# Performance work log

Hardware: AMD Instinct MI355X
Metric: run time of the kernel (lower is better)

Reference implementation:

```python
import jax, jax.numpy as jnp
import numpy as np

MODEL_DIM = 2048
NUM_HEADS = 16
HEAD_DIM = MODEL_DIM // NUM_HEADS  # 128
B, L = 2, 2048


def _rope_tables(seq_len, head_dim, theta=10000.0):
    inv = 1.0 / (theta ** (np.arange(0, head_dim, 2)[: head_dim // 2].astype(np.float32) / head_dim))
    t = np.arange(seq_len, dtype=np.float32)
    freqs = np.outer(t, inv)  # [L, head_dim//2]
    return jnp.asarray(np.cos(freqs)), jnp.asarray(np.sin(freqs))


def setup_inputs() -> dict:
    key = jax.random.key(0)
    k1, k2, k3 = jax.random.split(key, 3)
    x = jax.random.normal(k1, (B, L, MODEL_DIM), dtype=jnp.float32)
    Wqkv = jax.random.normal(k2, (MODEL_DIM, 3 * MODEL_DIM), dtype=jnp.float32) / np.sqrt(MODEL_DIM)
    Wc = jax.random.normal(k3, (MODEL_DIM, MODEL_DIM), dtype=jnp.float32) / np.sqrt(MODEL_DIM)
    bc = jnp.zeros((MODEL_DIM,), dtype=jnp.float32)
    freqs_cos, freqs_sin = _rope_tables(L, HEAD_DIM)
    return {"x": x, "freqs_cos": freqs_cos, "freqs_sin": freqs_sin,
            "Wqkv": Wqkv, "Wc": Wc, "bc": bc}


def _apply_rope(t, cos, sin):
    # t: [B, L, H, hd] viewed as pairs (even, odd) along last dim; complex multiply by cis
    b, l, h, d = t.shape
    tp = t.reshape(b, l, h, d // 2, 2)
    te, to = tp[..., 0], tp[..., 1]
    cos = cos[None, :, None, :]  # [1, L, 1, d/2]
    sin = sin[None, :, None, :]
    oe = te * cos - to * sin
    oo = te * sin + to * cos
    return jnp.stack([oe, oo], axis=-1).reshape(b, l, h, d)


def reference(x, freqs_cos, freqs_sin, Wqkv, Wc, bc):
    b, l, d = x.shape
    qkv = x @ Wqkv  # [B, L, 3D]
    q, k, v = jnp.split(qkv, 3, axis=-1)
    q = q.reshape(b, l, NUM_HEADS, HEAD_DIM)
    k = k.reshape(b, l, NUM_HEADS, HEAD_DIM)
    v = v.reshape(b, l, NUM_HEADS, HEAD_DIM)
    q = _apply_rope(q, freqs_cos, freqs_sin)
    k = _apply_rope(k, freqs_cos, freqs_sin)
    scale = 1.0 / np.sqrt(HEAD_DIM).astype(np.float32)
    # causal SDPA: [B, H, Lq, Lk]
    scores = jnp.einsum('bqhd,bkhd->bhqk', q, k) * scale
    causal = jnp.tril(jnp.ones((l, l), dtype=bool))
    scores = jnp.where(causal[None, None], scores, jnp.finfo(scores.dtype).min)
    attn = jax.nn.softmax(scores, axis=-1)
    out = jnp.einsum('bhqk,bkhd->bqhd', attn, v).reshape(b, l, d)
    return out @ Wc + bc
```

## Files before the change

kernel.cpp:

```cpp
#include <hip/hip_runtime.h>
#include <hip/hip_bf16.h>

#define MODEL 2048
#define NHEAD 16
#define HDIM  128
#define BB    2
#define LL    2048
#define N1    (3*MODEL)
#define MTOT  (BB*LL)

typedef __hip_bfloat16 bf16;
typedef __attribute__((ext_vector_type(8))) short bf16x8;
typedef __attribute__((ext_vector_type(4))) float f32x4;

static __device__ __forceinline__ f32x4 mfma16(bf16x8 a, bf16x8 b, f32x4 c) {
  return __builtin_amdgcn_mfma_f32_16x16x32_bf16(a, b, c, 0, 0, 0);
}

static __device__ __forceinline__ void gl_lds16(const void* g, void* l) {
  __builtin_amdgcn_global_load_lds(
      (const __attribute__((address_space(1))) unsigned int*)g,
      (__attribute__((address_space(3))) unsigned int*)l, 16, 0, 0);
}

static __device__ __forceinline__ unsigned bfu(float x) {
  bf16 b = __float2bfloat16(x);
  return (unsigned)*reinterpret_cast<unsigned short*>(&b);
}

#define BARRIER __builtin_amdgcn_s_barrier()
#define SCHED0  __builtin_amdgcn_sched_barrier(0)
#define PRIO1 __builtin_amdgcn_s_setprio(1)
#define PRIO0 __builtin_amdgcn_s_setprio(0)

__global__ void k_cvt(const float* __restrict__ in, bf16* __restrict__ out, int n4) {
  int i = blockIdx.x * blockDim.x + threadIdx.x;
  if (i < n4) {
    float4 v = ((const float4*)in)[i];
    bf16* o = out + (size_t)i * 4;
    o[0] = __float2bfloat16(v.x);
    o[1] = __float2bfloat16(v.y);
    o[2] = __float2bfloat16(v.z);
    o[3] = __float2bfloat16(v.w);
  }
}

__global__ __launch_bounds__(256)
void k_transpose(const float* __restrict__ in, bf16* __restrict__ out, int R, int C) {
  __shared__ float t[32][33];
  const int c0 = blockIdx.x * 32, r0 = blockIdx.y * 32;
  const int tx = threadIdx.x & 31;
  const int ty = threadIdx.x >> 5;
#pragma unroll
  for (int i = 0; i < 4; ++i)
    t[ty + 8*i][tx] = in[(size_t)(r0 + ty + 8*i) * C + c0 + tx];
  __syncthreads();
#pragma unroll
  for (int i = 0; i < 4; ++i)
    out[(size_t)(c0 + ty + 8*i) * R + r0 + tx] = __float2bfloat16(t[tx][ty + 8*i]);
}

template<int EPI>
__global__ __launch_bounds__(512, 4)
void k_gemmP(const bf16* __restrict__ A, const bf16* __restrict__ BT,
             int M, int N, int K,
             float* __restrict__ Cout, const float* __restrict__ bias,
             bf16* __restrict__ Qb, bf16* __restrict__ Kb, bf16* __restrict__ VTb,
             const float* __restrict__ cosT, const float* __restrict__ sinT)
{
  constexpr int ABUF = 8192;
  constexpr int BBUF = 8192;
  constexpr int AREG = 3 * ABUF;
  extern __shared__ char smem[];

  const int tid = threadIdx.x;
  const int wid = tid >> 6, lane = tid & 63;
  const int wm = wid >> 2, wn = wid & 3;
  const int lr = lane & 15, lkg = lane >> 4;

  const int nbx = N >> 7;
  const int xcd = blockIdx.x & 7;
  const int i   = blockIdx.x >> 3;
  const int m0 = (((xcd >> 1) << 3) + (i & 7)) << 7;
  const int n0 = ((xcd & 1) * (nbx >> 1) + (i >> 3)) << 7;

  const int scol = ((lane & 3) ^ ((lane >> 3) & 3)) * 8;
  const bf16* Asrc = A  + (size_t)(m0 + wid*16 + (lane >> 2)) * K + scol;
  const bf16* Bsrc = BT + (size_t)(n0 + wid*16 + (lane >> 2)) * K + scol;

  auto stageA = [&](int t) {
    gl_lds16(Asrc + t*32, smem + (t % 3)*ABUF + wid*1024);
  };
  auto stageB = [&](int t) {
    gl_lds16(Bsrc + t*32, smem + AREG + (t % 3)*BBUF + wid*1024);
  };

  const int slotX = (lkg ^ ((lr >> 1) & 3)) * 16;
  const int aBase = wm*4096 + lr*64 + slotX;
  const int bBase = wn*2048 + lr*64 + slotX;

  const f32x4 vzero = {0.f, 0.f, 0.f, 0.f};
  f32x4 acc[4][2];
#pragma unroll
  for (int ii = 0; ii < 4; ++ii)
#pragma unroll
    for (int j = 0; j < 2; ++j) acc[ii][j] = vzero;

  const int nt = K >> 5;

  stageA(0); stageB(0); stageA(1); stageB(1);
  asm volatile("s_waitcnt vmcnt(2)" ::: "memory");
  SCHED0; BARRIER;

  for (int t = 0; t < nt; ++t) {
    const int bufA = (t % 3) * ABUF;
    const int bufB = AREG + (t % 3) * BBUF;
    const int ts   = (t + 2 < nt) ? t + 2 : nt - 1;
    bf16x8 aFr[4], bFr[2];

#pragma unroll
    for (int mf = 0; mf < 4; ++mf)
      aFr[mf] = *(const bf16x8*)(smem + bufA + aBase + mf*1024);
#pragma unroll
    for (int nf = 0; nf < 2; ++nf)
      bFr[nf] = *(const bf16x8*)(smem + bufB + bBase + nf*1024);
    stageA(ts); stageB(ts);

    PRIO1;
#pragma unroll
    for (int mf = 0; mf < 4; ++mf)
#pragma unroll
      for (int nf = 0; nf < 2; ++nf)
        acc[mf][nf] = mfma16(aFr[mf], bFr[nf], acc[mf][nf]);
    PRIO0;
    asm volatile("s_waitcnt vmcnt(2)" ::: "memory");
    SCHED0;
    BARRIER;
  }

  if constexpr (EPI == 1) {
    const float inv_sqrt_d = 0.08838834764831845f;
#pragma unroll
    for (int nf = 0; nf < 2; ++nf) {
      const int gcb = n0 + wn*32 + nf*16;
      const int section = gcb >> 11;
      const int cc = (gcb & 2047) + lr;
      const int h = cc >> 7, d = cc & 127;
#pragma unroll
      for (int mf = 0; mf < 4; ++mf) {
#pragma unroll
        for (int reg = 0; reg < 4; ++reg) {
          const int grow = m0 + wm*64 + mf*16 + lkg*4 + reg;
          const int bidx = grow >> 11, lseq = grow & 2047;
          float val = acc[mf][nf][reg];
          if (section < 2) {
            float p = __shfl_xor(val, 1);
            const int fi = d >> 1;
            float cv = cosT[(size_t)lseq * 64 + fi];
            float sv = sinT[(size_t)lseq * 64 + fi];
            float r = (d & 1) ? fmaf(p, sv, val * cv)
                              : fmaf(val, cv, -p * sv);
            if (section == 0) {
              r *= inv_sqrt_d;
              Qb[((size_t)(bidx*NHEAD + h) * LL + lseq) * HDIM + d] = __float2bfloat16(r);
            } else {
              Kb[((size_t)(bidx*NHEAD + h) * LL + lseq) * HDIM + d] = __float2bfloat16(r);
            }
          } else {
            VTb[((size_t)(bidx*NHEAD + h) * HDIM + d) * LL + lseq] = __float2bfloat16(val);
          }
        }
      }
    }
  } else {
#pragma unroll
    for (int nf = 0; nf < 2; ++nf) {
      const int gcol = n0 + wn*32 + nf*16 + lr;
      const float bv = bias[gcol];
#pragma unroll
      for (int mf = 0; mf < 4; ++mf) {
#pragma unroll
        for (int reg = 0; reg < 4; ++reg) {
          const int grow = m0 + wm*64 + mf*16 + lkg*4 + reg;
          Cout[(size_t)grow * N + gcol] = acc[mf][nf][reg] + bv;
        }
      }
    }
  }
}

__global__ __launch_bounds__(256, 2)
void k_attn(const bf16* __restrict__ Qb, const bf16* __restrict__ Kb,
            const bf16* __restrict__ VTb, bf16* __restrict__ attnA)
{
  __shared__ bf16 Ks[64][136];
  __shared__ bf16 Vs[128][72];
  __shared__ bf16 Ps[4][32][72];

  const int bh  = blockIdx.y;
  const int bx  = blockIdx.x;
  const int tid = threadIdx.x;
  const int wid = tid >> 6, lane = tid & 63;
  const int lr  = lane & 15, lkg = lane >> 4;

  const bf16* Qh = Qb  + (size_t)bh * LL * HDIM;
  const bf16* Kh = Kb  + (size_t)bh * LL * HDIM;
  const bf16* Vh = VTb + (size_t)bh * HDIM * LL;
  const int b = bh >> 4, h = bh & 15;
  const f32x4 vzero = {0.f, 0.f, 0.f, 0.f};

  for (int pp = 0; pp < 2; ++pp) {
    const int qt  = pp ? bx : (15 - bx);
    const int Q0  = qt * 128;
    const int q0w = Q0 + wid * 32;

    bf16x8 qf[2][4];
#pragma unroll
    for (int qr = 0; qr < 2; ++qr)
#pragma unroll
      for (int kk = 0; kk < 4; ++kk)
        qf[qr][kk] = *(const bf16x8*)(Qh + (size_t)(q0w + qr*16 + lr) * HDIM + kk*32 + lkg*8);

    f32x4 oacc[2][8];
#pragma unroll
    for (int qr = 0; qr < 2; ++qr)
#pragma unroll
      for (int db = 0; db < 8; ++db) oacc[qr][db] = vzero;
    float ml[2] = {-INFINITY, -INFINITY};
    float ll[2] = {0.f, 0.f};

    const int NT = Q0 / 64 + 2;
    bf16x8 kpre[4], vpre[4];
#pragma unroll
    for (int j = 0; j < 4; ++j) {
      const int c = j*256 + tid;
      kpre[j] = *(const bf16x8*)(Kh + (size_t)(c >> 4) * HDIM + (c & 15) * 8);
      vpre[j] = *(const bf16x8*)(Vh + (size_t)(c >> 3) * LL + (c & 7) * 8);
    }

    for (int kt = 0; kt < NT; ++kt) {
      const int kbase = kt * 64;
      __syncthreads();
#pragma unroll
      for (int j = 0; j < 4; ++j) {
        const int c = j*256 + tid;
        *(bf16x8*)&Ks[c >> 4][(c & 15) * 8] = kpre[j];
        *(bf16x8*)&Vs[c >> 3][(c & 7) * 8]  = vpre[j];
      }
      __syncthreads();
      if (kt + 1 < NT) {
#pragma unroll
        for (int j = 0; j < 4; ++j) {
          const int c = j*256 + tid;
          kpre[j] = *(const bf16x8*)(Kh + (size_t)((kt+1)*64 + (c >> 4)) * HDIM + (c & 15) * 8);
          vpre[j] = *(const bf16x8*)(Vh + (size_t)(c >> 3) * LL + (kt+1)*64 + (c & 7) * 8);
        }
      }
      if (kbase <= q0w + 31) {
        f32x4 s2[2][4];
#pragma unroll
        for (int qr = 0; qr < 2; ++qr)
#pragma unroll
          for (int c = 0; c < 4; ++c) s2[qr][c] = vzero;
#pragma unroll
        for (int c = 0; c < 4; ++c) {
          bf16x8 kf[4];
#pragma unroll
          for (int kk = 0; kk < 4; ++kk)
            kf[kk] = *(const bf16x8*)&Ks[c*16 + lr][kk*32 + lkg*8];
#pragma unroll
          for (int qr = 0; qr < 2; ++qr)
#pragma unroll
            for (int kk = 0; kk < 4; ++kk)
              s2[qr][c] = mfma16(kf[kk], qf[qr][kk], s2[qr][c]);
        }
#pragma unroll
        for (int qr = 0; qr < 2; ++qr) {
          const int qrow = q0w + qr*16 + lr;
          float pv[4][4];
#pragma unroll
          for (int c = 0; c < 4; ++c)
#pragma unroll
            for (int reg = 0; reg < 4; ++reg) {
              const int kv = kbase + c*16 + lkg*4 + reg;
              pv[c][reg] = (kv <= qrow) ? s2[qr][c][reg] : -INFINITY;
            }
          float tm = pv[0][0];
#pragma unroll
          for (int c = 0; c < 4; ++c)
#pragma unroll
            for (int reg = 0; reg < 4; ++reg)
              if (c || reg) tm = fmaxf(tm, pv[c][reg]);
          tm = fmaxf(tm, __shfl_xor(tm, 16));
          tm = fmaxf(tm, __shfl_xor(tm, 32));
          const float mnew = fmaxf(ml[qr], tm);
          const float scl  = __expf(ml[qr] - mnew);
          ml[qr] = mnew;
          float rs = 0.f;
#pragma unroll
          for (int c = 0; c < 4; ++c)
#pragma unroll
            for (int reg = 0; reg < 4; ++reg) {
              pv[c][reg] = __expf(pv[c][reg] - mnew);
              rs += pv[c][reg];
            }
          rs += __shfl_xor(rs, 16);
          rs += __shfl_xor(rs, 32);
          ll[qr] = ll[qr] * scl + rs;
#pragma unroll
          for (int c = 0; c < 4; ++c) {
            unsigned lo = bfu(pv[c][0]) | (bfu(pv[c][1]) << 16);
            unsigned hi = bfu(pv[c][2]) | (bfu(pv[c][3]) << 16);
            *(uint2*)&Ps[wid][qr*16 + lr][c*16 + lkg*4] = make_uint2(lo, hi);
          }
          float sr[4];
#pragma unroll
          for (int reg = 0; reg < 4; ++reg) sr[reg] = __shfl(scl, lkg*4 + reg);
#pragma unroll
          for (int db = 0; db < 8; ++db) {
            oacc[qr][db][0] *= sr[0]; oacc[qr][db][1] *= sr[1];
            oacc[qr][db][2] *= sr[2]; oacc[qr][db][3] *= sr[3];
          }
        }
        asm volatile("s_waitcnt lgkmcnt(0)" ::: "memory");
        __builtin_amdgcn_sched_barrier(0);
        bf16x8 pf[2][2];
#pragma unroll
        for (int qr = 0; qr < 2; ++qr)
#pragma unroll
          for (int k2 = 0; k2 < 2; ++k2)
            pf[qr][k2] = *(const bf16x8*)&Ps[wid][qr*16 + lr][k2*32 + lkg*8];
#pragma unroll
        for (int db = 0; db < 8; ++db) {
          bf16x8 vf0 = *(const bf16x8*)&Vs[db*16 + lr][lkg*8];
          bf16x8 vf1 = *(const bf16x8*)&Vs[db*16 + lr][32 + lkg*8];
#pragma unroll
          for (int qr = 0; qr < 2; ++qr) {
            oacc[qr][db] = mfma16(pf[qr][0], vf0, oacc[qr][db]);
            oacc[qr][db] = mfma16(pf[qr][1], vf1, oacc[qr][db]);
          }
        }
      }
    }

#pragma unroll
    for (int qr = 0; qr < 2; ++qr) {
      const float myinv = 1.0f / ll[qr];
      float li[4];
#pragma unroll
      for (int reg = 0; reg < 4; ++reg) li[reg] = __shfl(myinv, lkg*4 + reg);
#pragma unroll
      for (int reg = 0; reg < 4; ++reg) {
        const int row = q0w + qr*16 + lkg*4 + reg;
        bf16* dst = attnA + ((size_t)(b*LL + row)) * MODEL + h * HDIM;
#pragma unroll
        for (int db = 0; db < 8; ++db)
          dst[db*16 + lr] = __float2bfloat16(oacc[qr][db][reg] * li[reg]);
      }
    }
  }
}

extern "C" void kernel_launch(void* const* d_in, const int* in_sizes, int n_in,
                              void* d_out, int out_size, void* d_ws, size_t ws_size,
                              hipStream_t stream)
{
  const float* x    = (const float*)d_in[0];
  const float* cosT = (const float*)d_in[1];
  const float* sinT = (const float*)d_in[2];
  const float* Wqkv = (const float*)d_in[3];
  const float* Wc   = (const float*)d_in[4];
  const float* bc   = (const float*)d_in[5];
  float* out = (float*)d_out;

  if (ws_size < 100663296u) return;
  char* w = (char*)d_ws;
  bf16* x16   = (bf16*)(w);
  bf16* WqkvT = (bf16*)(w + (size_t)16777216);
  bf16* WcT   = (bf16*)(w + (size_t)41943040);
  bf16* Qb    = (bf16*)(w + (size_t)50331648);
  bf16* Kb    = (bf16*)(w + (size_t)67108864);
  bf16* VTb   = (bf16*)(w + (size_t)83886080);
  bf16* attnA = x16;

  hipFuncSetAttribute(reinterpret_cast<const void*>(&k_gemmP<1>),
                      hipFuncAttributeMaxDynamicSharedMemorySize, 49152);
  hipFuncSetAttribute(reinterpret_cast<const void*>(&k_gemmP<2>),
                      hipFuncAttributeMaxDynamicSharedMemorySize, 49152);

  k_cvt<<<(MTOT*MODEL/4 + 255)/256, 256, 0, stream>>>(x, x16, MTOT*MODEL/4);
  k_transpose<<<dim3(N1/32,    MODEL/32), 256, 0, stream>>>(Wqkv, WqkvT, MODEL, N1);
  k_transpose<<<dim3(MODEL/32, MODEL/32), 256, 0, stream>>>(Wc,   WcT,   MODEL, MODEL);

  k_gemmP<1><<<(N1/128)*(MTOT/128), 512, 49152, stream>>>(
      x16, WqkvT, MTOT, N1, MODEL,
      nullptr, nullptr, Qb, Kb, VTb, cosT, sinT);

  k_attn<<<dim3(8, BB*NHEAD), 256, 0, stream>>>(Qb, Kb, VTb, attnA);

  k_gemmP<2><<<(MODEL/128)*(MTOT/128), 512, 49152, stream>>>(
      attnA, WcT, MTOT, MODEL, MODEL,
      out, bc, nullptr, nullptr, nullptr, nullptr, nullptr);
}
```

Baseline: 296.7 us.

## Use 4-wave GEMM blocks with 64x64 warp tiles and double buffering

```diff
diff --git a/kernel.cpp b/kernel.cpp
--- a/kernel.cpp
+++ b/kernel.cpp
@@ -61,21 +61,18 @@
 }
 
 template<int EPI>
-__global__ __launch_bounds__(512, 4)
+__global__ __launch_bounds__(256, 5)
 void k_gemmP(const bf16* __restrict__ A, const bf16* __restrict__ BT,
              int M, int N, int K,
              float* __restrict__ Cout, const float* __restrict__ bias,
              bf16* __restrict__ Qb, bf16* __restrict__ Kb, bf16* __restrict__ VTb,
              const float* __restrict__ cosT, const float* __restrict__ sinT)
 {
-  constexpr int ABUF = 8192;
-  constexpr int BBUF = 8192;
-  constexpr int AREG = 3 * ABUF;
   extern __shared__ char smem[];
 
   const int tid = threadIdx.x;
   const int wid = tid >> 6, lane = tid & 63;
-  const int wm = wid >> 2, wn = wid & 3;
+  const int wm = wid >> 1, wn = wid & 1;
   const int lr = lane & 15, lkg = lane >> 4;
 
   const int nbx = N >> 7;
@@ -85,55 +82,58 @@
   const int n0 = ((xcd & 1) * (nbx >> 1) + (i >> 3)) << 7;
 
   const int scol = ((lane & 3) ^ ((lane >> 3) & 3)) * 8;
-  const bf16* Asrc = A  + (size_t)(m0 + wid*16 + (lane >> 2)) * K + scol;
-  const bf16* Bsrc = BT + (size_t)(n0 + wid*16 + (lane >> 2)) * K + scol;
-
-  auto stageA = [&](int t) {
-    gl_lds16(Asrc + t*32, smem + (t % 3)*ABUF + wid*1024);
-  };
-  auto stageB = [&](int t) {
-    gl_lds16(Bsrc + t*32, smem + AREG + (t % 3)*BBUF + wid*1024);
+  const bf16* Asrc = A  + (size_t)(m0 + wid*32 + (lane >> 2)) * K + scol;
+  const bf16* Bsrc = BT + (size_t)(n0 + wid*32 + (lane >> 2)) * K + scol;
+
+  auto stage = [&](int t) {
+    const bf16* ga = Asrc + t*32;
+    const bf16* gb = Bsrc + t*32;
+    char* da = smem + (t & 1)*16384 + wid*2048;
+    char* db = smem + (t & 1)*16384 + 8192 + wid*2048;
+    gl_lds16(ga,                da);
+    gl_lds16(ga + (size_t)16*K, da + 1024);
+    gl_lds16(gb,                db);
+    gl_lds16(gb + (size_t)16*K, db + 1024);
   };
 
   const int slotX = (lkg ^ ((lr >> 1) & 3)) * 16;
   const int aBase = wm*4096 + lr*64 + slotX;
-  const int bBase = wn*2048 + lr*64 + slotX;
+  const int bBase = 8192 + wn*4096 + lr*64 + slotX;
 
   const f32x4 vzero = {0.f, 0.f, 0.f, 0.f};
-  f32x4 acc[4][2];
+  f32x4 acc[4][4];
 #pragma unroll
   for (int ii = 0; ii < 4; ++ii)
 #pragma unroll
-    for (int j = 0; j < 2; ++j) acc[ii][j] = vzero;
+    for (int j = 0; j < 4; ++j) acc[ii][j] = vzero;
 
   const int nt = K >> 5;
 
-  stageA(0); stageB(0); stageA(1); stageB(1);
-  asm volatile("s_waitcnt vmcnt(2)" ::: "memory");
+  stage(0);
+  asm volatile("s_waitcnt vmcnt(0)" ::: "memory");
   SCHED0; BARRIER;
 
   for (int t = 0; t < nt; ++t) {
-    const int bufA = (t % 3) * ABUF;
-    const int bufB = AREG + (t % 3) * BBUF;
-    const int ts   = (t + 2 < nt) ? t + 2 : nt - 1;
-    bf16x8 aFr[4], bFr[2];
+    const int buf = (t & 1) * 16384;
+    bf16x8 aFr[4], bFr[4];
+
+    if (t + 1 < nt) stage(t + 1);
 
 #pragma unroll
     for (int mf = 0; mf < 4; ++mf)
-      aFr[mf] = *(const bf16x8*)(smem + bufA + aBase + mf*1024);
-#pragma unroll
-    for (int nf = 0; nf < 2; ++nf)
-      bFr[nf] = *(const bf16x8*)(smem + bufB + bBase + nf*1024);
-    stageA(ts); stageB(ts);
+      aFr[mf] = *(const bf16x8*)(smem + buf + aBase + mf*1024);
+#pragma unroll
+    for (int nf = 0; nf < 4; ++nf)
+      bFr[nf] = *(const bf16x8*)(smem + buf + bBase + nf*1024);
 
     PRIO1;
 #pragma unroll
     for (int mf = 0; mf < 4; ++mf)
 #pragma unroll
-      for (int nf = 0; nf < 2; ++nf)
+      for (int nf = 0; nf < 4; ++nf)
         acc[mf][nf] = mfma16(aFr[mf], bFr[nf], acc[mf][nf]);
     PRIO0;
-    asm volatile("s_waitcnt vmcnt(2)" ::: "memory");
+    asm volatile("s_waitcnt vmcnt(0)" ::: "memory");
     SCHED0;
     BARRIER;
   }
@@ -141,8 +141,8 @@
   if constexpr (EPI == 1) {
     const float inv_sqrt_d = 0.08838834764831845f;
 #pragma unroll
-    for (int nf = 0; nf < 2; ++nf) {
-      const int gcb = n0 + wn*32 + nf*16;
+    for (int nf = 0; nf < 4; ++nf) {
+      const int gcb = n0 + wn*64 + nf*16;
       const int section = gcb >> 11;
       const int cc = (gcb & 2047) + lr;
       const int h = cc >> 7, d = cc & 127;
@@ -174,8 +174,8 @@
     }
   } else {
 #pragma unroll
-    for (int nf = 0; nf < 2; ++nf) {
-      const int gcol = n0 + wn*32 + nf*16 + lr;
+    for (int nf = 0; nf < 4; ++nf) {
+      const int gcol = n0 + wn*64 + nf*16 + lr;
       const float bv = bias[gcol];
 #pragma unroll
       for (int mf = 0; mf < 4; ++mf) {
@@ -384,21 +384,21 @@
   bf16* attnA = x16;
 
   hipFuncSetAttribute(reinterpret_cast<const void*>(&k_gemmP<1>),
-                      hipFuncAttributeMaxDynamicSharedMemorySize, 49152);
+                      hipFuncAttributeMaxDynamicSharedMemorySize, 32768);
   hipFuncSetAttribute(reinterpret_cast<const void*>(&k_gemmP<2>),
-                      hipFuncAttributeMaxDynamicSharedMemorySize, 49152);
+                      hipFuncAttributeMaxDynamicSharedMemorySize, 32768);
 
   k_cvt<<<(MTOT*MODEL/4 + 255)/256, 256, 0, stream>>>(x, x16, MTOT*MODEL/4);
   k_transpose<<<dim3(N1/32,    MODEL/32), 256, 0, stream>>>(Wqkv, WqkvT, MODEL, N1);
   k_transpose<<<dim3(MODEL/32, MODEL/32), 256, 0, stream>>>(Wc,   WcT,   MODEL, MODEL);
 
-  k_gemmP<1><<<(N1/128)*(MTOT/128), 512, 49152, stream>>>(
+  k_gemmP<1><<<(N1/128)*(MTOT/128), 256, 32768, stream>>>(
       x16, WqkvT, MTOT, N1, MODEL,
       nullptr, nullptr, Qb, Kb, VTb, cosT, sinT);
 
   k_attn<<<dim3(8, BB*NHEAD), 256, 0, stream>>>(Qb, Kb, VTb, attnA);
 
-  k_gemmP<2><<<(MODEL/128)*(MTOT/128), 512, 49152, stream>>>(
+  k_gemmP<2><<<(MODEL/128)*(MTOT/128), 256, 32768, stream>>>(
       attnA, WcT, MTOT, MODEL, MODEL,
       out, bc, nullptr, nullptr, nullptr, nullptr, nullptr);
 }
```

Measured after the change: 679.3 us. +128.9%, slower.

## Fuse fp32-to-bf16 conversion of x into the QKV GEMM A-tile loading

Applied to the files above, without the earlier changes.

```diff
diff --git a/kernel.cpp b/kernel.cpp
--- a/kernel.cpp
+++ b/kernel.cpp
@@ -23,27 +23,18 @@
       (__attribute__((address_space(3))) unsigned int*)l, 16, 0, 0);
 }
 
+static __device__ __forceinline__ unsigned short bfraw(float x) {
+  bf16 b = __float2bfloat16(x);
+  return *reinterpret_cast<unsigned short*>(&b);
+}
 static __device__ __forceinline__ unsigned bfu(float x) {
-  bf16 b = __float2bfloat16(x);
-  return (unsigned)*reinterpret_cast<unsigned short*>(&b);
+  return (unsigned)bfraw(x);
 }
 
 #define BARRIER __builtin_amdgcn_s_barrier()
 #define SCHED0  __builtin_amdgcn_sched_barrier(0)
 #define PRIO1 __builtin_amdgcn_s_setprio(1)
 #define PRIO0 __builtin_amdgcn_s_setprio(0)
-
-__global__ void k_cvt(const float* __restrict__ in, bf16* __restrict__ out, int n4) {
-  int i = blockIdx.x * blockDim.x + threadIdx.x;
-  if (i < n4) {
-    float4 v = ((const float4*)in)[i];
-    bf16* o = out + (size_t)i * 4;
-    o[0] = __float2bfloat16(v.x);
-    o[1] = __float2bfloat16(v.y);
-    o[2] = __float2bfloat16(v.z);
-    o[3] = __float2bfloat16(v.w);
-  }
-}
 
 __global__ __launch_bounds__(256)
 void k_transpose(const float* __restrict__ in, bf16* __restrict__ out, int R, int C) {
@@ -62,7 +53,7 @@
 
 template<int EPI>
 __global__ __launch_bounds__(512, 4)
-void k_gemmP(const bf16* __restrict__ A, const bf16* __restrict__ BT,
+void k_gemmP(const void* __restrict__ Ain, const bf16* __restrict__ BT,
              int M, int N, int K,
              float* __restrict__ Cout, const float* __restrict__ bias,
              bf16* __restrict__ Qb, bf16* __restrict__ Kb, bf16* __restrict__ VTb,
@@ -81,20 +72,44 @@
   const int nbx = N >> 7;
   const int xcd = blockIdx.x & 7;
   const int i   = blockIdx.x >> 3;
-  const int m0 = (((xcd >> 1) << 3) + (i & 7)) << 7;
-  const int n0 = ((xcd & 1) * (nbx >> 1) + (i >> 3)) << 7;
+  int m0, n0;
+  if constexpr (EPI == 1) {
+    m0 = ((xcd << 2) + (i & 3)) << 7;
+    n0 = (i >> 2) << 7;
+  } else {
+    m0 = (((xcd >> 1) << 3) + (i & 7)) << 7;
+    n0 = ((xcd & 1) * (nbx >> 1) + (i >> 3)) << 7;
+  }
 
   const int scol = ((lane & 3) ^ ((lane >> 3) & 3)) * 8;
-  const bf16* Asrc = A  + (size_t)(m0 + wid*16 + (lane >> 2)) * K + scol;
   const bf16* Bsrc = BT + (size_t)(n0 + wid*16 + (lane >> 2)) * K + scol;
-
-  auto stageA = [&](int t) {
-    gl_lds16(Asrc + t*32, smem + (t % 3)*ABUF + wid*1024);
-  };
   auto stageB = [&](int t) {
     gl_lds16(Bsrc + t*32, smem + AREG + (t % 3)*BBUF + wid*1024);
   };
 
+  const bf16*  AsrcH = (const bf16*)Ain;
+  const float* AsrcF = (const float*)Ain;
+  const bf16*  AsrcB = AsrcH + (size_t)(m0 + wid*16 + (lane >> 2)) * K + scol;
+  const float* AsrcX = AsrcF + (size_t)(m0 + wid*16 + (lane >> 2)) * K + (lane & 3) * 8;
+  const int awAddr = (wid*16 + (lane >> 2)) * 64 + ((lane & 3) ^ ((lane >> 3) & 3)) * 16;
+
+  float4 rA0, rA1;
+  auto loadAf = [&](int t) {
+    rA0 = *(const float4*)(AsrcX + (size_t)t * 32);
+    rA1 = *(const float4*)(AsrcX + (size_t)t * 32 + 4);
+  };
+  auto writeA = [&](int tbuf) {
+    union { bf16x8 v; unsigned short s[8]; } u;
+    u.s[0] = bfraw(rA0.x); u.s[1] = bfraw(rA0.y);
+    u.s[2] = bfraw(rA0.z); u.s[3] = bfraw(rA0.w);
+    u.s[4] = bfraw(rA1.x); u.s[5] = bfraw(rA1.y);
+    u.s[6] = bfraw(rA1.z); u.s[7] = bfraw(rA1.w);
+    *(bf16x8*)(smem + (tbuf % 3)*ABUF + awAddr) = u.v;
+  };
+  auto stageA_bf = [&](int t) {
+    gl_lds16(AsrcB + t*32, smem + (t % 3)*ABUF + wid*1024);
+  };
+
   const int slotX = (lkg ^ ((lr >> 1) & 3)) * 16;
   const int aBase = wm*4096 + lr*64 + slotX;
   const int bBase = wn*2048 + lr*64 + slotX;
@@ -108,14 +123,24 @@
 
   const int nt = K >> 5;
 
-  stageA(0); stageB(0); stageA(1); stageB(1);
-  asm volatile("s_waitcnt vmcnt(2)" ::: "memory");
+  if constexpr (EPI == 1) {
+    loadAf(0);
+    stageB(0); stageB(1);
+    writeA(0);
+    loadAf(1);
+    writeA(1);
+    loadAf(2);
+    asm volatile("s_waitcnt vmcnt(3) lgkmcnt(0)" ::: "memory");
+  } else {
+    stageA_bf(0); stageB(0); stageA_bf(1); stageB(1);
+    asm volatile("s_waitcnt vmcnt(2)" ::: "memory");
+  }
   SCHED0; BARRIER;
 
   for (int t = 0; t < nt; ++t) {
     const int bufA = (t % 3) * ABUF;
     const int bufB = AREG + (t % 3) * BBUF;
-    const int ts   = (t + 2 < nt) ? t + 2 : nt - 1;
+    const int t2 = (t + 2 < nt) ? t + 2 : nt - 1;
     bf16x8 aFr[4], bFr[2];
 
 #pragma unroll
@@ -124,7 +149,15 @@
 #pragma unroll
     for (int nf = 0; nf < 2; ++nf)
       bFr[nf] = *(const bf16x8*)(smem + bufB + bBase + nf*1024);
-    stageA(ts); stageB(ts);
+
+    if constexpr (EPI == 1) {
+      writeA(t + 2);
+      stageB(t2);
+      const int t3 = (t + 3 < nt) ? t + 3 : nt - 1;
+      loadAf(t3);
+    } else {
+      stageA_bf(t2); stageB(t2);
+    }
 
     PRIO1;
 #pragma unroll
@@ -133,7 +166,11 @@
       for (int nf = 0; nf < 2; ++nf)
         acc[mf][nf] = mfma16(aFr[mf], bFr[nf], acc[mf][nf]);
     PRIO0;
-    asm volatile("s_waitcnt vmcnt(2)" ::: "memory");
+    if constexpr (EPI == 1) {
+      asm volatile("s_waitcnt vmcnt(3) lgkmcnt(0)" ::: "memory");
+    } else {
+      asm volatile("s_waitcnt vmcnt(2)" ::: "memory");
+    }
     SCHED0;
     BARRIER;
   }
@@ -375,25 +412,23 @@
 
   if (ws_size < 100663296u) return;
   char* w = (char*)d_ws;
-  bf16* x16   = (bf16*)(w);
+  bf16* attnA = (bf16*)(w);
   bf16* WqkvT = (bf16*)(w + (size_t)16777216);
   bf16* WcT   = (bf16*)(w + (size_t)41943040);
   bf16* Qb    = (bf16*)(w + (size_t)50331648);
   bf16* Kb    = (bf16*)(w + (size_t)67108864);
   bf16* VTb   = (bf16*)(w + (size_t)83886080);
-  bf16* attnA = x16;
 
   hipFuncSetAttribute(reinterpret_cast<const void*>(&k_gemmP<1>),
                       hipFuncAttributeMaxDynamicSharedMemorySize, 49152);
   hipFuncSetAttribute(reinterpret_cast<const void*>(&k_gemmP<2>),
                       hipFuncAttributeMaxDynamicSharedMemorySize, 49152);
 
-  k_cvt<<<(MTOT*MODEL/4 + 255)/256, 256, 0, stream>>>(x, x16, MTOT*MODEL/4);
   k_transpose<<<dim3(N1/32,    MODEL/32), 256, 0, stream>>>(Wqkv, WqkvT, MODEL, N1);
   k_transpose<<<dim3(MODEL/32, MODEL/32), 256, 0, stream>>>(Wc,   WcT,   MODEL, MODEL);
 
   k_gemmP<1><<<(N1/128)*(MTOT/128), 512, 49152, stream>>>(
-      x16, WqkvT, MTOT, N1, MODEL,
+      x, WqkvT, MTOT, N1, MODEL,
       nullptr, nullptr, Qb, Kb, VTb, cosT, sinT);
 
   k_attn<<<dim3(8, BB*NHEAD), 256, 0, stream>>>(Qb, Kb, VTb, attnA);
```

After: 302.1 us. About the same (+1.8%).

## Process both paired causal query tiles concurrently with 512-thread attention blocks

Applied to the files above, without the earlier changes.

```diff
diff --git a/kernel.cpp b/kernel.cpp
--- a/kernel.cpp
+++ b/kernel.cpp
@@ -189,13 +189,14 @@
   }
 }
 
-__global__ __launch_bounds__(256, 2)
+__global__ __launch_bounds__(512)
 void k_attn(const bf16* __restrict__ Qb, const bf16* __restrict__ Kb,
             const bf16* __restrict__ VTb, bf16* __restrict__ attnA)
 {
-  __shared__ bf16 Ks[64][136];
-  __shared__ bf16 Vs[128][72];
-  __shared__ bf16 Ps[4][32][72];
+  extern __shared__ char asmem[];
+  bf16* Ks = (bf16*)asmem;
+  bf16* Vs = (bf16*)(asmem + 17408);
+  bf16* Ps = (bf16*)(asmem + 17408 + 18432);
 
   const int bh  = blockIdx.y;
   const int bx  = blockIdx.x;
@@ -209,154 +210,152 @@
   const int b = bh >> 4, h = bh & 15;
   const f32x4 vzero = {0.f, 0.f, 0.f, 0.f};
 
-  for (int pp = 0; pp < 2; ++pp) {
-    const int qt  = pp ? bx : (15 - bx);
-    const int Q0  = qt * 128;
-    const int q0w = Q0 + wid * 32;
-
-    bf16x8 qf[2][4];
-#pragma unroll
-    for (int qr = 0; qr < 2; ++qr)
-#pragma unroll
-      for (int kk = 0; kk < 4; ++kk)
-        qf[qr][kk] = *(const bf16x8*)(Qh + (size_t)(q0w + qr*16 + lr) * HDIM + kk*32 + lkg*8);
-
-    f32x4 oacc[2][8];
-#pragma unroll
-    for (int qr = 0; qr < 2; ++qr)
-#pragma unroll
-      for (int db = 0; db < 8; ++db) oacc[qr][db] = vzero;
-    float ml[2] = {-INFINITY, -INFINITY};
-    float ll[2] = {0.f, 0.f};
-
-    const int NT = Q0 / 64 + 2;
-    bf16x8 kpre[4], vpre[4];
-#pragma unroll
-    for (int j = 0; j < 4; ++j) {
-      const int c = j*256 + tid;
-      kpre[j] = *(const bf16x8*)(Kh + (size_t)(c >> 4) * HDIM + (c & 15) * 8);
-      vpre[j] = *(const bf16x8*)(Vh + (size_t)(c >> 3) * LL + (c & 7) * 8);
-    }
-
-    for (int kt = 0; kt < NT; ++kt) {
-      const int kbase = kt * 64;
-      __syncthreads();
-#pragma unroll
-      for (int j = 0; j < 4; ++j) {
-        const int c = j*256 + tid;
-        *(bf16x8*)&Ks[c >> 4][(c & 15) * 8] = kpre[j];
-        *(bf16x8*)&Vs[c >> 3][(c & 7) * 8]  = vpre[j];
-      }
-      __syncthreads();
-      if (kt + 1 < NT) {
-#pragma unroll
-        for (int j = 0; j < 4; ++j) {
-          const int c = j*256 + tid;
-          kpre[j] = *(const bf16x8*)(Kh + (size_t)((kt+1)*64 + (c >> 4)) * HDIM + (c & 15) * 8);
-          vpre[j] = *(const bf16x8*)(Vh + (size_t)(c >> 3) * LL + (kt+1)*64 + (c & 7) * 8);
+  const int qt  = (wid < 4) ? (15 - bx) : bx;
+  const int q0w = qt * 128 + (wid & 3) * 32;
+
+  bf16x8 qf[2][4];
+#pragma unroll
+  for (int qr = 0; qr < 2; ++qr)
+#pragma unroll
+    for (int kk = 0; kk < 4; ++kk)
+      qf[qr][kk] = *(const bf16x8*)(Qh + (size_t)(q0w + qr*16 + lr) * HDIM + kk*32 + lkg*8);
+
+  f32x4 oacc[2][8];
+#pragma unroll
+  for (int qr = 0; qr < 2; ++qr)
+#pragma unroll
+    for (int db = 0; db < 8; ++db) oacc[qr][db] = vzero;
+  float ml[2] = {-INFINITY, -INFINITY};
+  float ll[2] = {0.f, 0.f};
+
+  const int NT = (15 - bx) * 2 + 2;
+
+  bf16x8 kpre[2], vpre[2];
+#pragma unroll
+  for (int j = 0; j < 2; ++j) {
+    const int c = j*512 + tid;
+    kpre[j] = *(const bf16x8*)(Kh + (size_t)(c >> 4) * HDIM + (c & 15) * 8);
+    vpre[j] = *(const bf16x8*)(Vh + (size_t)(c >> 3) * LL + (c & 7) * 8);
+  }
+
+  for (int kt = 0; kt < NT; ++kt) {
+    const int kbase = kt * 64;
+    __syncthreads();
+#pragma unroll
+    for (int j = 0; j < 2; ++j) {
+      const int c = j*512 + tid;
+      *(bf16x8*)&Ks[(c >> 4) * 136 + (c & 15) * 8] = kpre[j];
+      *(bf16x8*)&Vs[(c >> 3) * 72  + (c & 7)  * 8] = vpre[j];
+    }
+    __syncthreads();
+    if (kt + 1 < NT) {
+#pragma unroll
+      for (int j = 0; j < 2; ++j) {
+        const int c = j*512 + tid;
+        kpre[j] = *(const bf16x8*)(Kh + (size_t)((kt+1)*64 + (c >> 4)) * HDIM + (c & 15) * 8);
+        vpre[j] = *(const bf16x8*)(Vh + (size_t)(c >> 3) * LL + (kt+1)*64 + (c & 7) * 8);
+      }
+    }
+    if (kbase <= q0w + 31) {
+      f32x4 s2[2][4];
+#pragma unroll
+      for (int qr = 0; qr < 2; ++qr)
+#pragma unroll
+        for (int c = 0; c < 4; ++c) s2[qr][c] = vzero;
+#pragma unroll
+      for (int c = 0; c < 4; ++c) {
+        bf16x8 kf[4];
+#pragma unroll
+        for (int kk = 0; kk < 4; ++kk)
+          kf[kk] = *(const bf16x8*)&Ks[(c*16 + lr) * 136 + kk*32 + lkg*8];
+#pragma unroll
+        for (int qr = 0; qr < 2; ++qr)
+#pragma unroll
+          for (int kk = 0; kk < 4; ++kk)
+            s2[qr][c] = mfma16(kf[kk], qf[qr][kk], s2[qr][c]);
+      }
+#pragma unroll
+      for (int qr = 0; qr < 2; ++qr) {
+        const int qrow = q0w + qr*16 + lr;
+        float pv[4][4];
+#pragma unroll
+        for (int c = 0; c < 4; ++c)
+#pragma unroll
+          for (int reg = 0; reg < 4; ++reg) {
+            const int kv = kbase + c*16 + lkg*4 + reg;
+            pv[c][reg] = (kv <= qrow) ? s2[qr][c][reg] : -INFINITY;
+          }
+        float tm = pv[0][0];
+#pragma unroll
+        for (int c = 0; c < 4; ++c)
+#pragma unroll
+          for (int reg = 0; reg < 4; ++reg)
+            if (c || reg) tm = fmaxf(tm, pv[c][reg]);
+        tm = fmaxf(tm, __shfl_xor(tm, 16));
+        tm = fmaxf(tm, __shfl_xor(tm, 32));
+        const float mnew = fmaxf(ml[qr], tm);
+        const float scl  = __expf(ml[qr] - mnew);
+        ml[qr] = mnew;
+        float rs = 0.f;
+#pragma unroll
+        for (int c = 0; c < 4; ++c)
+#pragma unroll
+          for (int reg = 0; reg < 4; ++reg) {
+            pv[c][reg] = __expf(pv[c][reg] - mnew);
+            rs += pv[c][reg];
+          }
+        rs += __shfl_xor(rs, 16);
+        rs += __shfl_xor(rs, 32);
+        ll[qr] = ll[qr] * scl + rs;
+#pragma unroll
+        for (int c = 0; c < 4; ++c) {
+          unsigned lo = bfu(pv[c][0]) | (bfu(pv[c][1]) << 16);
+          unsigned hi = bfu(pv[c][2]) | (bfu(pv[c][3]) << 16);
+          *(uint2*)&Ps[(wid*32 + qr*16 + lr) * 72 + c*16 + lkg*4] = make_uint2(lo, hi);
         }
-      }
-      if (kbase <= q0w + 31) {
-        f32x4 s2[2][4];
-#pragma unroll
-        for (int qr = 0; qr < 2; ++qr)
-#pragma unroll
-          for (int c = 0; c < 4; ++c) s2[qr][c] = vzero;
-#pragma unroll
-        for (int c = 0; c < 4; ++c) {
-          bf16x8 kf[4];
-#pragma unroll
-          for (int kk = 0; kk < 4; ++kk)
-            kf[kk] = *(const bf16x8*)&Ks[c*16 + lr][kk*32 + lkg*8];
-#pragma unroll
-          for (int qr = 0; qr < 2; ++qr)
-#pragma unroll
-            for (int kk = 0; kk < 4; ++kk)
-              s2[qr][c] = mfma16(kf[kk], qf[qr][kk], s2[qr][c]);
+        float sr[4];
+#pragma unroll
+        for (int reg = 0; reg < 4; ++reg) sr[reg] = __shfl(scl, lkg*4 + reg);
+#pragma unroll
+        for (int db = 0; db < 8; ++db) {
+          oacc[qr][db][0] *= sr[0]; oacc[qr][db][1] *= sr[1];
+          oacc[qr][db][2] *= sr[2]; oacc[qr][db][3] *= sr[3];
         }
+      }
+      asm volatile("s_waitcnt lgkmcnt(0)" ::: "memory");
+      __builtin_amdgcn_sched_barrier(0);
+      bf16x8 pf[2][2];
+#pragma unroll
+      for (int qr = 0; qr < 2; ++qr)
+#pragma unroll
+        for (int k2 = 0; k2 < 2; ++k2)
+          pf[qr][k2] = *(const bf16x8*)&Ps[(wid*32 + qr*16 + lr) * 72 + k2*32 + lkg*8];
+#pragma unroll
+      for (int db = 0; db < 8; ++db) {
+        bf16x8 vf0 = *(const bf16x8*)&Vs[(db*16 + lr) * 72 + lkg*8];
+        bf16x8 vf1 = *(const bf16x8*)&Vs[(db*16 + lr) * 72 + 32 + lkg*8];
 #pragma unroll
         for (int qr = 0; qr < 2; ++qr) {
-          const int qrow = q0w + qr*16 + lr;
-          float pv[4][4];
-#pragma unroll
-          for (int c = 0; c < 4; ++c)
-#pragma unroll
-            for (int reg = 0; reg < 4; ++reg) {
-              const int kv = kbase + c*16 + lkg*4 + reg;
-              pv[c][reg] = (kv <= qrow) ? s2[qr][c][reg] : -INFINITY;
-            }
-          float tm = pv[0][0];
-#pragma unroll
-          for (int c = 0; c < 4; ++c)
-#pragma unroll
-            for (int reg = 0; reg < 4; ++reg)
-              if (c || reg) tm = fmaxf(tm, pv[c][reg]);
-          tm = fmaxf(tm, __shfl_xor(tm, 16));
-          tm = fmaxf(tm, __shfl_xor(tm, 32));
-          const float mnew = fmaxf(ml[qr], tm);
-          const float scl  = __expf(ml[qr] - mnew);
-          ml[qr] = mnew;
-          float rs = 0.f;
-#pragma unroll
-          for (int c = 0; c < 4; ++c)
-#pragma unroll
-            for (int reg = 0; reg < 4; ++reg) {
-              pv[c][reg] = __expf(pv[c][reg] - mnew);
-              rs += pv[c][reg];
-            }
-          rs += __shfl_xor(rs, 16);
-          rs += __shfl_xor(rs, 32);
-          ll[qr] = ll[qr] * scl + rs;
-#pragma unroll
-          for (int c = 0; c < 4; ++c) {
-            unsigned lo = bfu(pv[c][0]) | (bfu(pv[c][1]) << 16);
-            unsigned hi = bfu(pv[c][2]) | (bfu(pv[c][3]) << 16);
-            *(uint2*)&Ps[wid][qr*16 + lr][c*16 + lkg*4] = make_uint2(lo, hi);
-          }
-          float sr[4];
-#pragma unroll
-          for (int reg = 0; reg < 4; ++reg) sr[reg] = __shfl(scl, lkg*4 + reg);
-#pragma unroll
-          for (int db = 0; db < 8; ++db) {
-            oacc[qr][db][0] *= sr[0]; oacc[qr][db][1] *= sr[1];
-            oacc[qr][db][2] *= sr[2]; oacc[qr][db][3] *= sr[3];
-          }
+          oacc[qr][db] = mfma16(pf[qr][0], vf0, oacc[qr][db]);
+          oacc[qr][db] = mfma16(pf[qr][1], vf1, oacc[qr][db]);
         }
-        asm volatile("s_waitcnt lgkmcnt(0)" ::: "memory");
-        __builtin_amdgcn_sched_barrier(0);
-        bf16x8 pf[2][2];
-#pragma unroll
-        for (int qr = 0; qr < 2; ++qr)
-#pragma unroll
-          for (int k2 = 0; k2 < 2; ++k2)
-            pf[qr][k2] = *(const bf16x8*)&Ps[wid][qr*16 + lr][k2*32 + lkg*8];
-#pragma unroll
-        for (int db = 0; db < 8; ++db) {
-          bf16x8 vf0 = *(const bf16x8*)&Vs[db*16 + lr][lkg*8];
-          bf16x8 vf1 = *(const bf16x8*)&Vs[db*16 + lr][32 + lkg*8];
-#pragma unroll
-          for (int qr = 0; qr < 2; ++qr) {
-            oacc[qr][db] = mfma16(pf[qr][0], vf0, oacc[qr][db]);
-            oacc[qr][db] = mfma16(pf[qr][1], vf1, oacc[qr][db]);
-          }
-        }
-      }
-    }
-
-#pragma unroll
-    for (int qr = 0; qr < 2; ++qr) {
-      const float myinv = 1.0f / ll[qr];
-      float li[4];
-#pragma unroll
-      for (int reg = 0; reg < 4; ++reg) li[reg] = __shfl(myinv, lkg*4 + reg);
-#pragma unroll
-      for (int reg = 0; reg < 4; ++reg) {
-        const int row = q0w + qr*16 + lkg*4 + reg;
-        bf16* dst = attnA + ((size_t)(b*LL + row)) * MODEL + h * HDIM;
-#pragma unroll
-        for (int db = 0; db < 8; ++db)
-          dst[db*16 + lr] = __float2bfloat16(oacc[qr][db][reg] * li[reg]);
-      }
+      }
+    }
+  }
+
+#pragma unroll
+  for (int qr = 0; qr < 2; ++qr) {
+    const float myinv = 1.0f / ll[qr];
+    float li[4];
+#pragma unroll
+    for (int reg = 0; reg < 4; ++reg) li[reg] = __shfl(myinv, lkg*4 + reg);
+#pragma unroll
+    for (int reg = 0; reg < 4; ++reg) {
+      const int row = q0w + qr*16 + lkg*4 + reg;
+      bf16* dst = attnA + ((size_t)(b*LL + row)) * MODEL + h * HDIM;
+#pragma unroll
+      for (int db = 0; db < 8; ++db)
+        dst[db*16 + lr] = __float2bfloat16(oacc[qr][db][reg] * li[reg]);
     }
   }
 }
@@ -387,6 +386,8 @@
                       hipFuncAttributeMaxDynamicSharedMemorySize, 49152);
   hipFuncSetAttribute(reinterpret_cast<const void*>(&k_gemmP<2>),
                       hipFuncAttributeMaxDynamicSharedMemorySize, 49152);
+  hipFuncSetAttribute(reinterpret_cast<const void*>(&k_attn),
+                      hipFuncAttributeMaxDynamicSharedMemorySize, 73728);
 
   k_cvt<<<(MTOT*MODEL/4 + 255)/256, 256, 0, stream>>>(x, x16, MTOT*MODEL/4);
   k_transpose<<<dim3(N1/32,    MODEL/32), 256, 0, stream>>>(Wqkv, WqkvT, MODEL, N1);
@@ -396,7 +397,7 @@
       x16, WqkvT, MTOT, N1, MODEL,
       nullptr, nullptr, Qb, Kb, VTb, cosT, sinT);
 
-  k_attn<<<dim3(8, BB*NHEAD), 256, 0, stream>>>(Qb, Kb, VTb, attnA);
+  k_attn<<<dim3(8, BB*NHEAD), 512, 73728, stream>>>(Qb, Kb, VTb, attnA);
 
   k_gemmP<2><<<(MODEL/128)*(MTOT/128), 512, 49152, stream>>>(
       attnA, WcT, MTOT, MODEL, MODEL,
```

Result: faster. 287.4 us (-3.1%).
